# Kernel optimization log

Hardware: AMD Instinct MI355X
Metric: run time of the kernel (lower is better)

The kernel has to match this reference:

```python
import jax, jax.numpy as jnp
import numpy as np

BOUNDS = [0.01, 1.0, 100.0]
STEPS = [128, 128]
ALPHA_C = 0.01          # cfg.renderer.alpha
N_IMPORTANCE = 128      # cfg.renderer.importance_steps
N_RAYS = 65536


def _zvals_log_coarse():
    # matches torch.linspace(log10(b[i]), log10(b[i+1]) - seg/steps[i], steps[i]) per segment
    segs = []
    for i, s in enumerate(STEPS):
        lo = np.log10(BOUNDS[i]); hi = np.log10(BOUNDS[i + 1])
        segs.append(np.linspace(lo, hi - (hi - lo) / s, s, dtype=np.float32))
    return np.concatenate(segs)


def _seg_scale():
    tot = float(sum(STEPS))
    return np.concatenate([np.full(s, s / tot, dtype=np.float32) for s in STEPS])


def setup_inputs() -> dict:
    key = jax.random.key(0)
    k1, k2, k3, k4 = jax.random.split(key, 4)
    sigmas_coarse = jax.random.uniform(k1, (N_RAYS, sum(STEPS)), dtype=jnp.float32) * 5.0
    sigmas_fine = jax.random.uniform(k2, (N_RAYS, N_IMPORTANCE), dtype=jnp.float32) * 5.0
    rgbs_fine = jax.random.uniform(k3, (N_RAYS, N_IMPORTANCE, 3), dtype=jnp.float32)
    bg_color = jax.random.uniform(k4, (3,), dtype=jnp.float32)
    return {"sigmas_coarse": sigmas_coarse, "sigmas_fine": sigmas_fine,
            "rgbs_fine": rgbs_fine, "bg_color": bg_color}


def _weights_from_sigmas(sigmas, z_log):
    # delta[:, :-1] = diff(z_log), last delta = 0 (as in efficient_sampling)
    delta = jnp.concatenate([z_log[:, 1:] - z_log[:, :-1], jnp.zeros_like(z_log[:, :1])], -1)
    alpha = 1.0 - jnp.exp(-sigmas * delta)
    alpha_shift = jnp.concatenate([jnp.zeros_like(alpha[:, :1]), alpha[:, :-1]], -1)
    trans = jnp.cumprod(1.0 - alpha_shift, axis=-1)   # transmittance
    return alpha * trans


def _reweight(weights):
    # pad with zeros, 3-tap max blur, floor by alpha/S, per-segment rescale, normalize
    wpad = jnp.pad(weights, ((0, 0), (1, 1)))
    w = 0.5 * (jnp.maximum(wpad[:, :-2], wpad[:, 1:-1]) + jnp.maximum(wpad[:, 1:-1], wpad[:, 2:]))
    w = w + ALPHA_C / w.shape[-1]
    w = w * jnp.asarray(_seg_scale())
    return w / jnp.sum(w, axis=-1, keepdims=True)


def _sample_pdf(bins, weights, n_samples):
    # weights already normalized -> pdf; deterministic stratified u for reproducibility
    cdf = jnp.cumsum(weights, axis=-1)                     # [N, S]
    u = (jnp.arange(n_samples, dtype=bins.dtype) + 0.5) / n_samples
    u = jnp.broadcast_to(u, (bins.shape[0], n_samples))    # [N, n]
    inds = jax.vmap(lambda c, uu: jnp.searchsorted(c, uu, side='right'))(cdf, u)
    S = bins.shape[-1]
    below = jnp.clip(inds - 1, 0, S - 1)
    above = jnp.clip(inds, 0, S - 1)
    cdf_b = jnp.take_along_axis(cdf, below, -1)
    cdf_a = jnp.take_along_axis(cdf, above, -1)
    bin_b = jnp.take_along_axis(bins, below, -1)
    bin_a = jnp.take_along_axis(bins, above, -1)
    denom = jnp.where(cdf_a - cdf_b < 1e-5, 1.0, cdf_a - cdf_b)
    t = (u - cdf_b) / denom
    return bin_b + t * (bin_a - bin_b)


def reference(sigmas_coarse, sigmas_fine, rgbs_fine, bg_color):
    # --- efficient_sampling (no_grad path) ---
    z_log = jnp.broadcast_to(jnp.asarray(_zvals_log_coarse()), sigmas_coarse.shape)
    w_coarse = _weights_from_sigmas(sigmas_coarse, z_log)
    w_re = _reweight(w_coarse)
    z_log_fine = _sample_pdf(z_log, w_re, N_IMPORTANCE)     # [N, n_imp], sorted
    z_fine = jnp.power(10.0, z_log_fine)
    # --- render_rays_log-style compositing on fine samples ---
    w_fine = _weights_from_sigmas(sigmas_fine, z_log_fine)
    image = jnp.einsum('ns,nsc->nc', w_fine, rgbs_fine)
    image = image + (1.0 - jnp.sum(w_fine, -1)[..., None]) * bg_color
    invdepth = jnp.sum(w_fine / z_fine, axis=-1)
    lo = np.float32(np.log10(BOUNDS[0])); hi = np.float32(np.log10(BOUNDS[-1]))
    z_log_s = (z_log_fine - lo) / (hi - lo)
    return image, invdepth, w_fine, z_log_s
```

## Files before the change

### kernel.cpp

```cpp
#include <hip/hip_runtime.h>

#define SC 256
#define NF 128

template<int CTRL, int RM, int BM>
__device__ __forceinline__ float dpp_add(float x) {
    int s = __builtin_amdgcn_update_dpp(0, __float_as_int(x), CTRL, RM, BM, true);
    return x + __int_as_float(s);
}
template<int CTRL>
__device__ __forceinline__ float dpp_mov0(float x) {
    return __int_as_float(__builtin_amdgcn_update_dpp(0, __float_as_int(x), CTRL, 0xF, 0xF, true));
}
__device__ __forceinline__ float lane_f(float x, int l) {
    return __int_as_float(__builtin_amdgcn_readlane(__float_as_int(x), l));
}

__device__ __forceinline__ float wave_incl_scan(float x) {
    x = dpp_add<0x111, 0xF, 0xF>(x);
    x = dpp_add<0x112, 0xF, 0xF>(x);
    x = dpp_add<0x114, 0xF, 0xF>(x);
    x = dpp_add<0x118, 0xF, 0xF>(x);
    x = dpp_add<0x142, 0xA, 0xF>(x);
    x = dpp_add<0x143, 0xC, 0xF>(x);
    return x;
}

__device__ __forceinline__ float wave_sum_lane0(float x) {
    x = dpp_add<0xB1, 0xF, 0xF>(x);
    x = dpp_add<0x4E, 0xF, 0xF>(x);
    x = dpp_add<0x124, 0xF, 0xF>(x);
    x = dpp_add<0x128, 0xF, 0xF>(x);
    return x + lane_f(x, 16) + lane_f(x, 32) + lane_f(x, 48);
}

__device__ __forceinline__ void scatter_bin(float* __restrict__ zbuf,
                                            int j, float cl, float cr) {
    int klo = (int)ceilf(fmaf(128.0f, cl, -0.5f));
    int khi = (int)ceilf(fmaf(128.0f, cr, -0.5f));
    if (klo < 0)  klo = 0;
    if (khi > NF) khi = NF;
    if (klo >= khi) return;
    float dn   = cr - cl;
    float invd = (dn < 1e-5f) ? 1.0f : __builtin_amdgcn_rcpf(dn);
    float scale = (j == 0) ? 0.0f : 0.015625f;
    float zL    = (j == 0) ? -2.0f : fmaf((float)(j - 1), 0.015625f, -2.0f);
    for (int k = klo; k < khi; ++k) {
        float u = ((float)k + 0.5f) * 0.0078125f;
        zbuf[k] = fmaf((u - cl) * invd, scale, zL);
    }
}

__global__ __launch_bounds__(256) void nerf_render_kernel(
    const float* __restrict__ sig_c,
    const float* __restrict__ sig_f,
    const float* __restrict__ rgb_f,
    const float* __restrict__ bg,
    float* __restrict__ out,
    int n_rays)
{
    const int lane = threadIdx.x & 63;
    const int wid  = threadIdx.x >> 6;
    const int ray  = (blockIdx.x << 2) + wid;
    if (ray >= n_rays) return;

    __shared__ float s_z[4][NF];

    const float4 sc4 = *reinterpret_cast<const float4*>(sig_c + (size_t)ray * SC + 4 * lane);
    const float2 sf  = *reinterpret_cast<const float2*>(sig_f + (size_t)ray * NF + 2 * lane);
    const float2* rp = reinterpret_cast<const float2*>(rgb_f + (size_t)ray * (NF * 3) + 6 * lane);
    const float2 ra = rp[0], rb = rp[1], rc = rp[2];
    const float bg0 = bg[0], bg1 = bg[1], bg2 = bg[2];

    const float DLT = 0.015625f;
    float x0 = sc4.x * DLT;
    float x1 = sc4.y * DLT;
    float x2 = sc4.z * DLT;
    float x3 = (lane == 63) ? 0.0f : sc4.w * DLT;

    float p0 = x0, p1 = p0 + x1, p2 = p1 + x2, p3 = p2 + x3;
    float incl = wave_incl_scan(p3);
    float excl = incl - p3;

    float T0 = __expf(-excl);
    float T1 = __expf(-(excl + p0));
    float T2 = __expf(-(excl + p1));
    float T3 = __expf(-(excl + p2));
    float T4 = __expf(-(excl + p3));
    float w0 = T0 - T1, w1 = T1 - T2, w2 = T2 - T3, w3 = T3 - T4;

    float wl = dpp_mov0<0x138>(w3);
    float wr = dpp_mov0<0x130>(w0);

    const float FLOOR = 0.01f / 256.0f;
    float m01 = fmaxf(w0, w1), m12 = fmaxf(w1, w2), m23 = fmaxf(w2, w3);
    float r0 = 0.5f * (fmaxf(wl, w0) + m01) + FLOOR;
    float r1 = 0.5f * (m01 + m12) + FLOOR;
    float r2 = 0.5f * (m12 + m23) + FLOOR;
    float r3 = 0.5f * (m23 + fmaxf(w3, wr)) + FLOOR;

    float q0 = r0, q1 = q0 + r1, q2 = q1 + r2, q3 = q2 + r3;
    float incl2 = wave_incl_scan(q3);
    float excl2 = incl2 - q3;
    float total = lane_f(incl2, 63);
    float inv_total = __builtin_amdgcn_rcpf(total);

    float c0 = (excl2 + q0) * inv_total;
    float c1 = (excl2 + q1) * inv_total;
    float c2 = (excl2 + q2) * inv_total;
    float c3 = (excl2 + q3) * inv_total;
    float cprev = dpp_mov0<0x138>(c3);

    float* zbuf = s_z[wid];
    const int jb = 4 * lane;
    scatter_bin(zbuf, jb + 0, cprev, c0);
    scatter_bin(zbuf, jb + 1, c0,    c1);
    scatter_bin(zbuf, jb + 2, c1,    c2);
    scatter_bin(zbuf, jb + 3, c2,    c3);

    __asm__ __volatile__("" ::: "memory");

    const float2 zl2 = *reinterpret_cast<const float2*>(&zbuf[2 * lane]);
    float zl0 = zl2.x, zl1 = zl2.y;

    float znext = dpp_mov0<0x130>(zl0);
    float d0 = zl1 - zl0;
    float d1 = (lane == 63) ? 0.0f : (znext - zl1);

    float y0 = sf.x * d0;
    float y1 = sf.y * d1;
    float ps = y0 + y1;
    float fincl = wave_incl_scan(ps);
    float fexcl = fincl - ps;

    float U0 = __expf(-fexcl);
    float U1 = __expf(-(fexcl + y0));
    float U2 = __expf(-(fexcl + ps));
    float wf0 = U0 - U1, wf1 = U1 - U2;

    float img_r = wf0 * ra.x + wf1 * rb.y;
    float img_g = wf0 * ra.y + wf1 * rc.x;
    float img_b = wf0 * rb.x + wf1 * rc.y;
    float wsum  = wf0 + wf1;
    float invd = wf0 * __exp10f(-zl0) + wf1 * __exp10f(-zl1);

    img_r = wave_sum_lane0(img_r);
    img_g = wave_sum_lane0(img_g);
    img_b = wave_sum_lane0(img_b);
    wsum  = wave_sum_lane0(wsum);
    invd  = wave_sum_lane0(invd);

    float* out_img  = out;
    float* out_invd = out + (size_t)n_rays * 3;
    float* out_wf   = out + (size_t)n_rays * 4;
    float* out_zs   = out + (size_t)n_rays * 4 + (size_t)n_rays * NF;

    if (lane == 0) {
        float one_m = 1.0f - wsum;
        out_img[(size_t)ray * 3 + 0] = img_r + one_m * bg0;
        out_img[(size_t)ray * 3 + 1] = img_g + one_m * bg1;
        out_img[(size_t)ray * 3 + 2] = img_b + one_m * bg2;
        out_invd[ray] = invd;
    }
    *reinterpret_cast<float2*>(out_wf + (size_t)ray * NF + 2 * lane) =
        make_float2(wf0, wf1);
    *reinterpret_cast<float2*>(out_zs + (size_t)ray * NF + 2 * lane) =
        make_float2((zl0 + 2.0f) * 0.25f, (zl1 + 2.0f) * 0.25f);
}

extern "C" void kernel_launch(void* const* d_in, const int* in_sizes, int n_in,
                              void* d_out, int out_size, void* d_ws, size_t ws_size,
                              hipStream_t stream) {
    const float* sig_c = (const float*)d_in[0];
    const float* sig_f = (const float*)d_in[1];
    const float* rgb_f = (const float*)d_in[2];
    const float* bg    = (const float*)d_in[3];
    float* out = (float*)d_out;

    const int n_rays = in_sizes[1] / NF;
    dim3 grid((n_rays + 3) / 4), block(256);
    hipLaunchKernelGGL(nerf_render_kernel, grid, block, 0, stream,
                       sig_c, sig_f, rgb_f, bg, out, n_rays);
}
```

Before: 237.8 us.

## Replace per-bin sample scatter loop with bin-start markers and wave max-scan

```diff
diff --git a/kernel.cpp b/kernel.cpp
--- a/kernel.cpp
+++ b/kernel.cpp
@@ -7,6 +7,11 @@
 __device__ __forceinline__ float dpp_add(float x) {
     int s = __builtin_amdgcn_update_dpp(0, __float_as_int(x), CTRL, RM, BM, true);
     return x + __int_as_float(s);
+}
+template<int CTRL, int RM, int BM>
+__device__ __forceinline__ int dpp_imax(int x) {
+    int s = __builtin_amdgcn_update_dpp(0, x, CTRL, RM, BM, true);
+    return (x > s) ? x : s;
 }
 template<int CTRL>
 __device__ __forceinline__ float dpp_mov0(float x) {
@@ -26,6 +31,16 @@
     return x;
 }
 
+__device__ __forceinline__ int wave_incl_scan_imax(int x) {
+    x = dpp_imax<0x111, 0xF, 0xF>(x);
+    x = dpp_imax<0x112, 0xF, 0xF>(x);
+    x = dpp_imax<0x114, 0xF, 0xF>(x);
+    x = dpp_imax<0x118, 0xF, 0xF>(x);
+    x = dpp_imax<0x142, 0xA, 0xF>(x);
+    x = dpp_imax<0x143, 0xC, 0xF>(x);
+    return x;
+}
+
 __device__ __forceinline__ float wave_sum_lane0(float x) {
     x = dpp_add<0xB1, 0xF, 0xF>(x);
     x = dpp_add<0x4E, 0xF, 0xF>(x);
@@ -34,21 +49,9 @@
     return x + lane_f(x, 16) + lane_f(x, 32) + lane_f(x, 48);
 }
 
-__device__ __forceinline__ void scatter_bin(float* __restrict__ zbuf,
-                                            int j, float cl, float cr) {
-    int klo = (int)ceilf(fmaf(128.0f, cl, -0.5f));
-    int khi = (int)ceilf(fmaf(128.0f, cr, -0.5f));
-    if (klo < 0)  klo = 0;
-    if (khi > NF) khi = NF;
-    if (klo >= khi) return;
-    float dn   = cr - cl;
-    float invd = (dn < 1e-5f) ? 1.0f : __builtin_amdgcn_rcpf(dn);
-    float scale = (j == 0) ? 0.0f : 0.015625f;
-    float zL    = (j == 0) ? -2.0f : fmaf((float)(j - 1), 0.015625f, -2.0f);
-    for (int k = klo; k < khi; ++k) {
-        float u = ((float)k + 0.5f) * 0.0078125f;
-        zbuf[k] = fmaf((u - cl) * invd, scale, zL);
-    }
+__device__ __forceinline__ int bin_klo(float c) {
+    int k = (int)ceilf(fmaf(128.0f, c, -0.5f));
+    return (k < 0) ? 0 : k;
 }
 
 __global__ __launch_bounds__(256) void nerf_render_kernel(
@@ -64,7 +67,8 @@
     const int ray  = (blockIdx.x << 2) + wid;
     if (ray >= n_rays) return;
 
-    __shared__ float s_z[4][NF];
+    __shared__ float s_cdf[4][SC];
+    __shared__ int   s_idx[4][NF];
 
     const float4 sc4 = *reinterpret_cast<const float4*>(sig_c + (size_t)ray * SC + 4 * lane);
     const float2 sf  = *reinterpret_cast<const float2*>(sig_f + (size_t)ray * NF + 2 * lane);
@@ -111,17 +115,49 @@
     float c3 = (excl2 + q3) * inv_total;
     float cprev = dpp_mov0<0x138>(c3);
 
-    float* zbuf = s_z[wid];
+    float* cdf = s_cdf[wid];
+    int*   idx = s_idx[wid];
+
+    *reinterpret_cast<float4*>(&cdf[4 * lane]) = make_float4(c0, c1, c2, c3);
+
+    *reinterpret_cast<int2*>(&idx[2 * lane]) = make_int2(-1, -1);
+
     const int jb = 4 * lane;
-    scatter_bin(zbuf, jb + 0, cprev, c0);
-    scatter_bin(zbuf, jb + 1, c0,    c1);
-    scatter_bin(zbuf, jb + 2, c1,    c2);
-    scatter_bin(zbuf, jb + 3, c2,    c3);
+    int k0 = bin_klo(cprev);
+    int k1 = bin_klo(c0);
+    int k2 = bin_klo(c1);
+    int k3 = bin_klo(c2);
+    int k4 = bin_klo(c3);
+    if (k0 < k1 && k0 < NF) idx[k0] = jb + 0;
+    if (k1 < k2 && k1 < NF) idx[k1] = jb + 1;
+    if (k2 < k3 && k2 < NF) idx[k2] = jb + 2;
+    if (k3 < k4 && k3 < NF) idx[k3] = jb + 3;
 
     __asm__ __volatile__("" ::: "memory");
 
-    const float2 zl2 = *reinterpret_cast<const float2*>(&zbuf[2 * lane]);
-    float zl0 = zl2.x, zl1 = zl2.y;
+    const int2 jraw = *reinterpret_cast<const int2*>(&idx[2 * lane]);
+    int m  = (jraw.x > jraw.y) ? jraw.x : jraw.y;
+    int M  = wave_incl_scan_imax(m);
+    int E  = __builtin_amdgcn_update_dpp(0, M, 0x138, 0xF, 0xF, true);
+    int j0 = (E  > jraw.x) ? E  : jraw.x;
+    int j1 = (j0 > jraw.y) ? j0 : jraw.y;
+
+    int b0 = (j0 > 0) ? j0 - 1 : 0;
+    int b1 = (j1 > 0) ? j1 - 1 : 0;
+    float ca0 = cdf[j0], cb0 = cdf[b0];
+    float ca1 = cdf[j1], cb1 = cdf[b1];
+
+    const float u0 = ((float)(2 * lane) + 0.5f) * 0.0078125f;
+    const float u1 = ((float)(2 * lane) + 1.5f) * 0.0078125f;
+
+    float dn0 = ca0 - cb0;  dn0 = (dn0 < 1e-5f) ? 1.0f : dn0;
+    float dn1 = ca1 - cb1;  dn1 = (dn1 < 1e-5f) ? 1.0f : dn1;
+    float sc0f = (j0 > 0) ? DLT : 0.0f;
+    float sc1f = (j1 > 0) ? DLT : 0.0f;
+    float zL0 = fmaf((float)b0, DLT, -2.0f);
+    float zL1 = fmaf((float)b1, DLT, -2.0f);
+    float zl0 = fmaf((u0 - cb0) * __builtin_amdgcn_rcpf(dn0), sc0f, zL0);
+    float zl1 = fmaf((u1 - cb1) * __builtin_amdgcn_rcpf(dn1), sc1f, zL1);
 
     float znext = dpp_mov0<0x130>(zl0);
     float d0 = zl1 - zl0;
```

Result: no change. 236.3 us (-0.6%).
